# Performance work log

Measured on AMD Instinct MI355X. Metric: run time of the kernel, lower is better.

Reference implementation:

```python
import jax, jax.numpy as jnp
import numpy as np

N_NODES = 100000
N_EDGES = 3200000
DIMS = [3, 64, 64, 64, 128, 1024, 512, 256, 2]  # per GCNemb.__init__


def setup_inputs() -> dict:
    key = jax.random.key(0)
    ks = jax.random.split(key, 2 + 2 * 8)
    x = jax.random.normal(ks[0], (N_NODES, DIMS[0]), dtype=jnp.float32)
    edge_index = jax.random.randint(ks[1], (2, N_EDGES), 0, N_NODES, dtype=jnp.int64)
    inp = {"x": x, "edge_index": edge_index}
    for i in range(8):
        scale = 1.0 / np.sqrt(DIMS[i])
        inp[f"W{i}"] = jax.random.normal(ks[2 + 2 * i], (DIMS[i], DIMS[i + 1]), dtype=jnp.float32) * scale
        inp[f"b{i}"] = jnp.zeros((DIMS[i + 1],), dtype=jnp.float32)
    return inp


def _gcn_norm(edge_index, n):
    # PyG GCNConv default: add self-loops, symmetric normalization.
    loop = jnp.arange(n, dtype=edge_index.dtype)
    row = jnp.concatenate([edge_index[0], loop])  # source
    col = jnp.concatenate([edge_index[1], loop])  # target
    deg = jax.ops.segment_sum(jnp.ones_like(col, dtype=jnp.float32), col, num_segments=n)
    dinv = jnp.where(deg > 0, jax.lax.rsqrt(deg), 0.0)
    norm = dinv[row] * dinv[col]  # [E+N]
    return row, col, norm


def _gcn_conv(x, W, b, row, col, norm, n):
    h = x @ W  # [N, out]
    agg = jax.ops.segment_sum(h[row] * norm[:, None], col, num_segments=n)
    return agg + b


def reference(x, edge_index, W0, b0, W1, b1, W2, b2, W3, b3, W4, b4, W5, b5, W6, b6, W7, b7):
    n = x.shape[0]
    row, col, norm = _gcn_norm(edge_index, n)
    Ws = [W0, W1, W2, W3, W4, W5, W6, W7]
    bs = [b0, b1, b2, b3, b4, b5, b6, b7]
    for i in range(7):
        x = jax.nn.relu(_gcn_conv(x, Ws[i], bs[i], row, col, norm, n))
    return _gcn_conv(x, Ws[7], bs[7], row, col, norm, n)
```

## Files before the change

kernel.cpp:

```cpp
#include <hip/hip_runtime.h>
#include <hip/hip_bf16.h>
#include <cstdint>
#include <cstddef>


#define TPB 256
#define SI 8
#define STILE (TPB * SI)

typedef short short8 __attribute__((ext_vector_type(8)));
typedef float f32x4 __attribute__((ext_vector_type(4)));

__device__ __forceinline__ float b2f(unsigned short u) {
    union { unsigned int i; float f; } c; c.i = ((unsigned int)u) << 16; return c.f;
}
__device__ __forceinline__ unsigned short f2b(float f) {
    __hip_bfloat16 h = __float2bfloat16(f);
    union { __hip_bfloat16 h; unsigned short u; } c; c.h = h; return c.u;
}

__device__ __forceinline__ void async_copy16(void* lds, const void* g) {
    __builtin_amdgcn_global_load_lds(
        (const __attribute__((address_space(1))) void*)g,
        (__attribute__((address_space(3))) void*)lds,
        16, 0, 0);
}


__global__ void count_deg_kernel(const int* __restrict__ col, int* __restrict__ deg,
                                 int E, int n) {
    int e = blockIdx.x * blockDim.x + threadIdx.x;
    if (e < E) {
        int c = col[e];
        if ((unsigned)c < (unsigned)n) atomicAdd(&deg[c], 1);
    }
}

__global__ void dinv_kernel(const int* __restrict__ deg, float* __restrict__ dinv, int n) {
    int i = blockIdx.x * blockDim.x + threadIdx.x;
    if (i < n) dinv[i] = 1.0f / sqrtf((float)(deg[i] + 1));
}

__global__ __launch_bounds__(TPB) void scan_part1(const int* __restrict__ deg,
                                                  int* __restrict__ bsum, int n) {
    int t0 = blockIdx.x * STILE + threadIdx.x * SI;
    int s = 0;
#pragma unroll
    for (int j = 0; j < SI; j++) { int i = t0 + j; if (i < n) s += deg[i]; }
#pragma unroll
    for (int off = 32; off >= 1; off >>= 1) s += __shfl_xor(s, off);
    __shared__ int ws[TPB / 64];
    if ((threadIdx.x & 63) == 0) ws[threadIdx.x >> 6] = s;
    __syncthreads();
    if (threadIdx.x == 0) {
        int tot = 0;
        for (int i = 0; i < TPB / 64; i++) tot += ws[i];
        bsum[blockIdx.x] = tot;
    }
}

__global__ void scan_part2(int* __restrict__ bsum, int nb,
                           int* __restrict__ rowptr, int n) {
    __shared__ int sums[1024];
    int tid = threadIdx.x;
    int v = (tid < nb) ? bsum[tid] : 0;
    sums[tid] = v;
    __syncthreads();
    for (int off = 1; off < 1024; off <<= 1) {
        int t = (tid >= off) ? sums[tid - off] : 0;
        __syncthreads();
        sums[tid] += t;
        __syncthreads();
    }
    if (tid < nb) bsum[tid] = (tid == 0) ? 0 : sums[tid - 1];
    if (tid == 0) rowptr[n] = sums[1023];
}

__global__ __launch_bounds__(TPB) void scan_part3(const int* __restrict__ deg,
                                                  const int* __restrict__ bsum,
                                                  int* __restrict__ rowptr,
                                                  int* __restrict__ cursor, int n) {
    int tid = threadIdx.x;
    int lane = tid & 63, wv = tid >> 6;
    int t0 = blockIdx.x * STILE + tid * SI;
    int v[SI]; int s = 0;
#pragma unroll
    for (int j = 0; j < SI; j++) { int i = t0 + j; v[j] = (i < n) ? deg[i] : 0; s += v[j]; }
    int sc = s;
#pragma unroll
    for (int off = 1; off < 64; off <<= 1) {
        int t = __shfl_up(sc, off);
        if (lane >= off) sc += t;
    }
    __shared__ int wtot[TPB / 64];
    if (lane == 63) wtot[wv] = sc;
    __syncthreads();
    int woff = 0;
    for (int i = 0; i < wv; i++) woff += wtot[i];
    int off0 = bsum[blockIdx.x] + woff + (sc - s);
#pragma unroll
    for (int j = 0; j < SI; j++) {
        int i = t0 + j;
        if (i < n) { rowptr[i] = off0; cursor[i] = off0; }
        off0 += v[j];
    }
}

__global__ void fill_csr_kernel(const int* __restrict__ row, const int* __restrict__ col,
                                const float* __restrict__ dinv,
                                int* __restrict__ cursor, int2* __restrict__ es,
                                int E, int n) {
    int e = blockIdx.x * blockDim.x + threadIdx.x;
    if (e < E) {
        int c = col[e];
        if ((unsigned)c < (unsigned)n) {
            int r = row[e];
            int pos = atomicAdd(&cursor[c], 1);
            if ((unsigned)pos < (unsigned)E) {
                es[pos] = make_int2(r, __float_as_int(dinv[r]));
            }
        }
    }
}

__global__ void convert_wt_kernel(const float* __restrict__ W, unsigned short* __restrict__ Wt,
                                  int K, int M) {
    int idx = blockIdx.x * blockDim.x + threadIdx.x;
    if (idx < K * M) {
        int k = idx / M, m = idx % M;
        Wt[(size_t)m * K + k] = f2b(W[idx]);
    }
}


template <int VEC> struct Pack;
template <> struct Pack<1> { using T = unsigned short; };
template <> struct Pack<2> { using T = unsigned int; };
template <> struct Pack<4> { using T = uint2; };

template <int VEC>
__global__ __launch_bounds__(TPB) void agg_win_kernel(
        const unsigned short* __restrict__ x, unsigned short* __restrict__ out,
        const int* __restrict__ rowptr, const int2* __restrict__ es,
        const float* __restrict__ dinv, const float* __restrict__ bias,
        int n, int d, int wb, int relu) {
    using P = typename Pack<VEC>::T;
    int wid  = (blockIdx.x * blockDim.x + threadIdx.x) >> 6;
    int lane = threadIdx.x & 63;
    if (wid >= n) return;
    int start = rowptr[wid], end = rowptr[wid + 1];
    float acc0[VEC], acc1[VEC], acc2[VEC], acc3[VEC];
#pragma unroll
    for (int j = 0; j < VEC; j++) { acc0[j] = 0.f; acc1[j] = 0.f; acc2[j] = 0.f; acc3[j] = 0.f; }
    const int fo = wb + lane * VEC;
    union U { P v; unsigned short u[VEC]; };

    for (int base = start; base < end; base += 64) {
        int idx = base + lane;
        int clamped = (idx < end) ? idx : (end - 1);
        int2 ev = es[clamped];
        int   sv = ev.x;
        float dv = (idx < end) ? __int_as_float(ev.y) : 0.f;
        int cnt = end - base; if (cnt > 64) cnt = 64;
        int j = 0;
        for (; j + 4 <= cnt; j += 4) {
            int   s0 = __shfl(sv, j),     s1 = __shfl(sv, j + 1);
            int   s2 = __shfl(sv, j + 2), s3 = __shfl(sv, j + 3);
            float e0 = __shfl(dv, j),     e1 = __shfl(dv, j + 1);
            float e2 = __shfl(dv, j + 2), e3 = __shfl(dv, j + 3);
            U l0, l1, l2, l3;
            l0.v = *(const P*)(x + (size_t)s0 * d + fo);
            l1.v = *(const P*)(x + (size_t)s1 * d + fo);
            l2.v = *(const P*)(x + (size_t)s2 * d + fo);
            l3.v = *(const P*)(x + (size_t)s3 * d + fo);
#pragma unroll
            for (int q = 0; q < VEC; q++) {
                acc0[q] = fmaf(e0, b2f(l0.u[q]), acc0[q]);
                acc1[q] = fmaf(e1, b2f(l1.u[q]), acc1[q]);
                acc2[q] = fmaf(e2, b2f(l2.u[q]), acc2[q]);
                acc3[q] = fmaf(e3, b2f(l3.u[q]), acc3[q]);
            }
        }
        for (; j < cnt; j++) {
            int   s0 = __shfl(sv, j);
            float e0 = __shfl(dv, j);
            U l0; l0.v = *(const P*)(x + (size_t)s0 * d + fo);
#pragma unroll
            for (int q = 0; q < VEC; q++) acc0[q] = fmaf(e0, b2f(l0.u[q]), acc0[q]);
        }
    }

    float di = dinv[wid];
    U ls; ls.v = *(const P*)(x + (size_t)wid * d + fo);
    U st;
#pragma unroll
    for (int j = 0; j < VEC; j++) {
        float a = (acc0[j] + acc1[j]) + (acc2[j] + acc3[j]);
        float v = di * (a + di * b2f(ls.u[j]));
        if (bias) v += bias[fo + j];
        if (relu) v = fmaxf(v, 0.f);
        st.u[j] = f2b(v);
    }
    *(P*)(out + (size_t)wid * d + fo) = st.v;
}

__global__ __launch_bounds__(TPB) void agg_gemm64_kernel(
        const unsigned short* __restrict__ x, unsigned short* __restrict__ out,
        const int* __restrict__ rowptr, const int2* __restrict__ es,
        const float* __restrict__ dinv, const float* __restrict__ W,
        const float* __restrict__ bias, int n) {
    __shared__ float Ws[64 * 64];
    __shared__ float aggs[TPB / 64][64];
    const int tid = threadIdx.x;
    for (int i = tid; i < 64 * 64; i += TPB) Ws[i] = W[i];
    __syncthreads();
    int wid  = (blockIdx.x * TPB + tid) >> 6;
    int lane = tid & 63;
    int wv   = tid >> 6;
    if (wid >= n) return;
    int start = rowptr[wid], end = rowptr[wid + 1];
    float acc0 = 0.f, acc1 = 0.f, acc2 = 0.f, acc3 = 0.f;
    for (int base = start; base < end; base += 64) {
        int idx = base + lane;
        int clamped = (idx < end) ? idx : (end - 1);
        int2 ev = es[clamped];
        int   sv = ev.x;
        float dv = (idx < end) ? __int_as_float(ev.y) : 0.f;
        int cnt = end - base; if (cnt > 64) cnt = 64;
        int j = 0;
        for (; j + 4 <= cnt; j += 4) {
            int   s0 = __shfl(sv, j),     s1 = __shfl(sv, j + 1);
            int   s2 = __shfl(sv, j + 2), s3 = __shfl(sv, j + 3);
            float e0 = __shfl(dv, j),     e1 = __shfl(dv, j + 1);
            float e2 = __shfl(dv, j + 2), e3 = __shfl(dv, j + 3);
            acc0 = fmaf(e0, b2f(x[(size_t)s0 * 64 + lane]), acc0);
            acc1 = fmaf(e1, b2f(x[(size_t)s1 * 64 + lane]), acc1);
            acc2 = fmaf(e2, b2f(x[(size_t)s2 * 64 + lane]), acc2);
            acc3 = fmaf(e3, b2f(x[(size_t)s3 * 64 + lane]), acc3);
        }
        for (; j < cnt; j++) {
            int   s0 = __shfl(sv, j);
            float e0 = __shfl(dv, j);
            acc0 = fmaf(e0, b2f(x[(size_t)s0 * 64 + lane]), acc0);
        }
    }
    float di = dinv[wid];
    float a = di * (((acc0 + acc1) + (acc2 + acc3)) + di * b2f(x[(size_t)wid * 64 + lane]));
    aggs[wv][lane] = a;
    float v = bias[lane];
#pragma unroll 8
    for (int j = 0; j < 64; j++) v = fmaf(aggs[wv][j], Ws[j * 64 + lane], v);
    v = fmaxf(v, 0.f);
    out[(size_t)wid * 64 + lane] = f2b(v);
}

template <int D, int FUSE64>
__global__ __launch_bounds__(TPB) void agg_small_wave_kernel(
        const float* __restrict__ x, float* __restrict__ outf,
        unsigned short* __restrict__ outb,
        const int* __restrict__ rowptr, const int2* __restrict__ es,
        const float* __restrict__ dinv, const float* __restrict__ bias,
        const float* __restrict__ W, int n, int relu) {
    int wid  = (blockIdx.x * blockDim.x + threadIdx.x) >> 6;
    int lane = threadIdx.x & 63;
    if (wid >= n) return;
    int start = rowptr[wid], end = rowptr[wid + 1];
    float acc[D];
#pragma unroll
    for (int j = 0; j < D; j++) acc[j] = 0.f;
    for (int e = start + lane; e < end; e += 64) {
        int2 ev = es[e];
        int s = ev.x;
        float ds = __int_as_float(ev.y);
#pragma unroll
        for (int j = 0; j < D; j++) acc[j] = fmaf(ds, x[(size_t)s * D + j], acc[j]);
    }
#pragma unroll
    for (int j = 0; j < D; j++) {
#pragma unroll
        for (int off = 32; off >= 1; off >>= 1) acc[j] += __shfl_xor(acc[j], off);
    }
    float di = dinv[wid];
    float aggv[D];
#pragma unroll
    for (int j = 0; j < D; j++) aggv[j] = di * (acc[j] + di * x[(size_t)wid * D + j]);

    if (FUSE64) {
        float v = bias[lane];
#pragma unroll
        for (int j = 0; j < D; j++) v = fmaf(aggv[j], W[j * 64 + lane], v);
        v = fmaxf(v, 0.f);
        outb[(size_t)wid * 64 + lane] = f2b(v);
    } else {
        if (lane < D) {
            float v = aggv[lane];
            if (bias) v += bias[lane];
            if (relu) v = fmaxf(v, 0.f);
            outf[(size_t)wid * D + lane] = v;
        }
    }
}

__global__ __launch_bounds__(TPB) void gemm_dot2_kernel(
        const unsigned short* __restrict__ A, const float* __restrict__ W,
        float* __restrict__ pre, int n) {
    int wid  = (blockIdx.x * blockDim.x + threadIdx.x) >> 6;
    int lane = threadIdx.x & 63;
    if (wid >= n) return;
    union { uint2 v; unsigned short u[4]; } a;
    a.v = *(const uint2*)(A + (size_t)wid * 256 + lane * 4);
    float c0 = 0.f, c1 = 0.f;
#pragma unroll
    for (int j = 0; j < 4; j++) {
        float av = b2f(a.u[j]);
        c0 = fmaf(av, W[(lane * 4 + j) * 2 + 0], c0);
        c1 = fmaf(av, W[(lane * 4 + j) * 2 + 1], c1);
    }
#pragma unroll
    for (int off = 32; off >= 1; off >>= 1) {
        c0 += __shfl_xor(c0, off);
        c1 += __shfl_xor(c1, off);
    }
    if (lane == 0) { pre[(size_t)wid * 2 + 0] = c0; pre[(size_t)wid * 2 + 1] = c1; }
}

__global__ __launch_bounds__(256) void gemm_mfma_kernel(
        const unsigned short* __restrict__ A, const unsigned short* __restrict__ Wt,
        const float* __restrict__ bias, unsigned short* __restrict__ C,
        int nr, int K, int M, int relu, int addbias) {
    __shared__ alignas(16) short As[128 * 32];
    __shared__ alignas(16) short Bs[128 * 32];
    const int tid  = threadIdx.x;
    const int w    = tid >> 6;
    const int lane = tid & 63;
    const int wr   = w >> 1;
    const int wc   = w & 1;
    const int row0 = blockIdx.x * 128;
    const int col0 = blockIdx.y * 128;

    f32x4 acc[4][4];
#pragma unroll
    for (int i = 0; i < 4; i++)
#pragma unroll
        for (int j = 0; j < 4; j++) acc[i][j] = {0.f, 0.f, 0.f, 0.f};

    const int lrow   = lane >> 2;
    const int lcolB  = (lane & 3) * 16;
    const int fm     = lane & 15;
    const int fq     = lane >> 4;

    for (int kk = 0; kk < K; kk += 32) {
#pragma unroll
        for (int i = 0; i < 2; i++) {
            int r = w * 32 + i * 16 + lrow;
            int grow = row0 + r;
            const char* g = (const char*)A + ((size_t)grow * K + kk) * 2 + lcolB;
            short* lds = &As[(w * 32 + i * 16) * 32];
            if (grow < nr) async_copy16(lds, g);
        }
#pragma unroll
        for (int i = 0; i < 2; i++) {
            int r = w * 32 + i * 16 + lrow;
            int gcol = col0 + r;
            const char* g = (const char*)Wt + ((size_t)gcol * K + kk) * 2 + lcolB;
            short* lds = &Bs[(w * 32 + i * 16) * 32];
            async_copy16(lds, g);
        }
        __syncthreads();

        short8 a[4], b[4];
#pragma unroll
        for (int i = 0; i < 4; i++) {
            a[i] = *(const short8*)&As[(wr * 64 + i * 16 + fm) * 32 + fq * 8];
            b[i] = *(const short8*)&Bs[(wc * 64 + i * 16 + fm) * 32 + fq * 8];
        }
#pragma unroll
        for (int mi = 0; mi < 4; mi++)
#pragma unroll
            for (int ni = 0; ni < 4; ni++)
                acc[mi][ni] = __builtin_amdgcn_mfma_f32_16x16x32_bf16(
                    a[mi], b[ni], acc[mi][ni], 0, 0, 0);
        __syncthreads();
    }

#pragma unroll
    for (int mi = 0; mi < 4; mi++) {
#pragma unroll
        for (int r = 0; r < 4; r++) {
            int row = row0 + wr * 64 + mi * 16 + fq * 4 + r;
            if (row >= nr) continue;
            size_t rb = (size_t)row * M;
#pragma unroll
            for (int ni = 0; ni < 4; ni++) {
                int col = col0 + wc * 64 + ni * 16 + fm;
                float v = acc[mi][ni][r];
                if (addbias) v += bias[col];
                if (relu) v = fmaxf(v, 0.f);
                C[rb + col] = f2b(v);
            }
        }
    }
}

static inline void launch_gemm_mfma(const unsigned short* A, const unsigned short* Wt,
                                    const float* bias, unsigned short* C,
                                    int nr, int K, int M, int relu, int addbias,
                                    hipStream_t stream) {
    dim3 grid((nr + 127) / 128, M / 128);
    gemm_mfma_kernel<<<grid, 256, 0, stream>>>(A, Wt, bias, C, nr, K, M, relu, addbias);
}


static inline size_t al256(size_t x) { return (x + 255) & ~(size_t)255; }

extern "C" void kernel_launch(void* const* d_in, const int* in_sizes, int n_in,
                              void* d_out, int out_size, void* d_ws, size_t ws_size,
                              hipStream_t stream) {
    const float* x  = (const float*)d_in[0];
    const int*   ei = (const int*)d_in[1];
    const int E = in_sizes[1] / 2;
    const int n = in_sizes[0] / 3;
    const int* rowv = ei;
    const int* colv = ei + E;

    const float* Wf[8]; const float* bt[8];
    for (int i = 0; i < 8; i++) { Wf[i] = (const float*)d_in[2 + 2 * i]; bt[i] = (const float*)d_in[3 + 2 * i]; }

    char* p = (char*)d_ws;
    size_t used = 0;
    auto carve = [&](size_t bytes) -> char* {
        char* r = p + used; used += al256(bytes); return r;
    };
    int*   deg    = (int*)carve((size_t)n * 4);
    float* dinv   = (float*)carve((size_t)n * 4);
    int*   rowptr = (int*)carve((size_t)(n + 1) * 4);
    int*   cursor = (int*)carve((size_t)(n + 1) * 4);
    int*   bsum   = (int*)carve(4096 * 4);
    int2*  es     = (int2*)carve((size_t)E * 8);
    unsigned short* bufA = (unsigned short*)carve((size_t)n * 512 * 2);
    unsigned short* bufB = (unsigned short*)carve((size_t)n * 512 * 2);
    const size_t wt3e = 64 * 128, wt4e = 128 * 1024, wt5e = 1024 * 512, wt6e = 512 * 256;
    unsigned short* wt3 = (unsigned short*)carve((wt3e + wt4e + wt5e + wt6e) * 2);
    unsigned short* wt4 = wt3 + wt3e;
    unsigned short* wt5 = wt4 + wt4e;
    unsigned short* wt6 = wt5 + wt5e;
    size_t avail = (ws_size > used) ? (ws_size - used) : 0;
    int chunk = (int)(avail / (1024 * 2));
    if (chunk > n) chunk = n;
    chunk &= ~127;
    if (chunk < 2048) chunk = 2048;
    char* tmp_raw = carve((size_t)chunk * 1024 * 2);
    unsigned short* tmpb = (unsigned short*)tmp_raw;
    float* tmpf = (float*)tmp_raw;

    const int EB = (E + TPB - 1) / TPB;
    const int NB = (n + TPB - 1) / TPB;
    const int NW = (n + 3) / 4;
    const int SBK = (n + STILE - 1) / STILE;

    hipMemsetAsync(deg, 0, (size_t)n * 4, stream);
    count_deg_kernel<<<EB, TPB, 0, stream>>>(colv, deg, E, n);
    dinv_kernel<<<NB, TPB, 0, stream>>>(deg, dinv, n);
    scan_part1<<<SBK, TPB, 0, stream>>>(deg, bsum, n);
    scan_part2<<<1, 1024, 0, stream>>>(bsum, SBK, rowptr, n);
    scan_part3<<<SBK, TPB, 0, stream>>>(deg, bsum, rowptr, cursor, n);
    fill_csr_kernel<<<EB, TPB, 0, stream>>>(rowv, colv, dinv, cursor, es, E, n);

    convert_wt_kernel<<<(int)((wt3e + 255) / 256), 256, 0, stream>>>(Wf[3], wt3, 64, 128);
    convert_wt_kernel<<<(int)((wt4e + 255) / 256), 256, 0, stream>>>(Wf[4], wt4, 128, 1024);
    convert_wt_kernel<<<(int)((wt5e + 255) / 256), 256, 0, stream>>>(Wf[5], wt5, 1024, 512);
    convert_wt_kernel<<<(int)((wt6e + 255) / 256), 256, 0, stream>>>(Wf[6], wt6, 512, 256);

    agg_small_wave_kernel<3, 1><<<NW, TPB, 0, stream>>>(
        x, nullptr, bufA, rowptr, es, dinv, bt[0], Wf[0], n, 1);

    agg_gemm64_kernel<<<NW, TPB, 0, stream>>>(bufA, bufB, rowptr, es, dinv, Wf[1], bt[1], n);
    agg_gemm64_kernel<<<NW, TPB, 0, stream>>>(bufB, bufA, rowptr, es, dinv, Wf[2], bt[2], n);

    agg_win_kernel<1><<<NW, TPB, 0, stream>>>(bufA, bufB, rowptr, es, dinv, nullptr, n, 64, 0, 0);
    launch_gemm_mfma(bufB, wt3, bt[3], bufA, n, 64, 128, 1, 1, stream);

    agg_win_kernel<2><<<NW, TPB, 0, stream>>>(bufA, bufB, rowptr, es, dinv, nullptr, n, 128, 0, 0);
    for (int r0 = 0; r0 < n; r0 += chunk) {
        int ch = n - r0; if (ch > chunk) ch = chunk;
        launch_gemm_mfma(bufB + (size_t)r0 * 128, wt4, bt[4], tmpb, ch, 128, 1024, 1, 1, stream);
        launch_gemm_mfma(tmpb, wt5, nullptr, bufA + (size_t)r0 * 512, ch, 1024, 512, 0, 0, stream);
    }
    agg_win_kernel<4><<<NW, TPB, 0, stream>>>(bufA, bufB, rowptr, es, dinv, bt[5], n, 512, 0, 1);
    agg_win_kernel<4><<<NW, TPB, 0, stream>>>(bufA, bufB, rowptr, es, dinv, bt[5], n, 512, 256, 1);

    launch_gemm_mfma(bufB, wt6, nullptr, bufA, n, 512, 256, 0, 0, stream);
    agg_win_kernel<4><<<NW, TPB, 0, stream>>>(bufA, bufB, rowptr, es, dinv, bt[6], n, 256, 0, 1);

    gemm_dot2_kernel<<<NW, TPB, 0, stream>>>(bufB, Wf[7], tmpf, n);
    agg_small_wave_kernel<2, 0><<<NW, TPB, 0, stream>>>(
        tmpf, (float*)d_out, nullptr, rowptr, es, dinv, bt[7], nullptr, n, 0);
}
```

Measured before the change: 2.036 ms.

## Unroll aggregation gathers by 8, load GEMM B operand directly, narrow 512-dim windows

```diff
diff --git a/kernel.cpp b/kernel.cpp
--- a/kernel.cpp
+++ b/kernel.cpp
@@ -149,9 +149,11 @@
     int lane = threadIdx.x & 63;
     if (wid >= n) return;
     int start = rowptr[wid], end = rowptr[wid + 1];
-    float acc0[VEC], acc1[VEC], acc2[VEC], acc3[VEC];
-#pragma unroll
-    for (int j = 0; j < VEC; j++) { acc0[j] = 0.f; acc1[j] = 0.f; acc2[j] = 0.f; acc3[j] = 0.f; }
+    float acc[4][VEC];
+#pragma unroll
+    for (int g = 0; g < 4; g++)
+#pragma unroll
+        for (int j = 0; j < VEC; j++) acc[g][j] = 0.f;
     const int fo = wb + lane * VEC;
     union U { P v; unsigned short u[VEC]; };
 
@@ -163,30 +165,24 @@
         float dv = (idx < end) ? __int_as_float(ev.y) : 0.f;
         int cnt = end - base; if (cnt > 64) cnt = 64;
         int j = 0;
-        for (; j + 4 <= cnt; j += 4) {
-            int   s0 = __shfl(sv, j),     s1 = __shfl(sv, j + 1);
-            int   s2 = __shfl(sv, j + 2), s3 = __shfl(sv, j + 3);
-            float e0 = __shfl(dv, j),     e1 = __shfl(dv, j + 1);
-            float e2 = __shfl(dv, j + 2), e3 = __shfl(dv, j + 3);
-            U l0, l1, l2, l3;
-            l0.v = *(const P*)(x + (size_t)s0 * d + fo);
-            l1.v = *(const P*)(x + (size_t)s1 * d + fo);
-            l2.v = *(const P*)(x + (size_t)s2 * d + fo);
-            l3.v = *(const P*)(x + (size_t)s3 * d + fo);
-#pragma unroll
-            for (int q = 0; q < VEC; q++) {
-                acc0[q] = fmaf(e0, b2f(l0.u[q]), acc0[q]);
-                acc1[q] = fmaf(e1, b2f(l1.u[q]), acc1[q]);
-                acc2[q] = fmaf(e2, b2f(l2.u[q]), acc2[q]);
-                acc3[q] = fmaf(e3, b2f(l3.u[q]), acc3[q]);
-            }
+        for (; j + 8 <= cnt; j += 8) {
+            int s[8]; float e[8]; U l[8];
+#pragma unroll
+            for (int q = 0; q < 8; q++) { s[q] = __shfl(sv, j + q); e[q] = __shfl(dv, j + q); }
+#pragma unroll
+            for (int q = 0; q < 8; q++) l[q].v = *(const P*)(x + (size_t)s[q] * d + fo);
+#pragma unroll
+            for (int q = 0; q < 8; q++)
+#pragma unroll
+                for (int t = 0; t < VEC; t++)
+                    acc[q & 3][t] = fmaf(e[q], b2f(l[q].u[t]), acc[q & 3][t]);
         }
         for (; j < cnt; j++) {
             int   s0 = __shfl(sv, j);
             float e0 = __shfl(dv, j);
             U l0; l0.v = *(const P*)(x + (size_t)s0 * d + fo);
 #pragma unroll
-            for (int q = 0; q < VEC; q++) acc0[q] = fmaf(e0, b2f(l0.u[q]), acc0[q]);
+            for (int t = 0; t < VEC; t++) acc[0][t] = fmaf(e0, b2f(l0.u[t]), acc[0][t]);
         }
     }
 
@@ -195,7 +191,7 @@
     U st;
 #pragma unroll
     for (int j = 0; j < VEC; j++) {
-        float a = (acc0[j] + acc1[j]) + (acc2[j] + acc3[j]);
+        float a = (acc[0][j] + acc[1][j]) + (acc[2][j] + acc[3][j]);
         float v = di * (a + di * b2f(ls.u[j]));
         if (bias) v += bias[fo + j];
         if (relu) v = fmaxf(v, 0.f);
@@ -329,7 +325,6 @@
         const float* __restrict__ bias, unsigned short* __restrict__ C,
         int nr, int K, int M, int relu, int addbias) {
     __shared__ alignas(16) short As[128 * 32];
-    __shared__ alignas(16) short Bs[128 * 32];
     const int tid  = threadIdx.x;
     const int w    = tid >> 6;
     const int lane = tid & 63;
@@ -349,6 +344,11 @@
     const int fm     = lane & 15;
     const int fq     = lane >> 4;
 
+    const unsigned short* wtb[4];
+#pragma unroll
+    for (int i = 0; i < 4; i++)
+        wtb[i] = Wt + (size_t)(col0 + wc * 64 + i * 16 + fm) * K + fq * 8;
+
     for (int kk = 0; kk < K; kk += 32) {
 #pragma unroll
         for (int i = 0; i < 2; i++) {
@@ -358,22 +358,15 @@
             short* lds = &As[(w * 32 + i * 16) * 32];
             if (grow < nr) async_copy16(lds, g);
         }
-#pragma unroll
-        for (int i = 0; i < 2; i++) {
-            int r = w * 32 + i * 16 + lrow;
-            int gcol = col0 + r;
-            const char* g = (const char*)Wt + ((size_t)gcol * K + kk) * 2 + lcolB;
-            short* lds = &Bs[(w * 32 + i * 16) * 32];
-            async_copy16(lds, g);
-        }
+        short8 b[4];
+#pragma unroll
+        for (int i = 0; i < 4; i++) b[i] = *(const short8*)(wtb[i] + kk);
         __syncthreads();
 
-        short8 a[4], b[4];
-#pragma unroll
-        for (int i = 0; i < 4; i++) {
+        short8 a[4];
+#pragma unroll
+        for (int i = 0; i < 4; i++)
             a[i] = *(const short8*)&As[(wr * 64 + i * 16 + fm) * 32 + fq * 8];
-            b[i] = *(const short8*)&Bs[(wc * 64 + i * 16 + fm) * 32 + fq * 8];
-        }
 #pragma unroll
         for (int mi = 0; mi < 4; mi++)
 #pragma unroll
@@ -486,8 +479,9 @@
         launch_gemm_mfma(bufB + (size_t)r0 * 128, wt4, bt[4], tmpb, ch, 128, 1024, 1, 1, stream);
         launch_gemm_mfma(tmpb, wt5, nullptr, bufA + (size_t)r0 * 512, ch, 1024, 512, 0, 0, stream);
     }
-    agg_win_kernel<4><<<NW, TPB, 0, stream>>>(bufA, bufB, rowptr, es, dinv, bt[5], n, 512, 0, 1);
-    agg_win_kernel<4><<<NW, TPB, 0, stream>>>(bufA, bufB, rowptr, es, dinv, bt[5], n, 512, 256, 1);
+    for (int wpass = 0; wpass < 4; wpass++)
+        agg_win_kernel<2><<<NW, TPB, 0, stream>>>(
+            bufA, bufB, rowptr, es, dinv, bt[5], n, 512, wpass * 128, 1);
 
     launch_gemm_mfma(bufB, wt6, nullptr, bufA, n, 512, 256, 0, 0, stream);
     agg_win_kernel<4><<<NW, TPB, 0, stream>>>(bufA, bufB, rowptr, es, dinv, bt[6], n, 256, 0, 1);
```

New measurement: 2.212 ms. +8.6%, slower.
